# Optimization experiments

Measured on AMD Instinct MI355X. Metric: run time of the kernel, lower is better.

The kernel has to match this reference:

```python
import jax, jax.numpy as jnp
import numpy as np

N = 8192       # num nodes
D_IN = 256     # in_features
D_OUT = 128    # out_features per head
H = 2          # num_heads
E = 262144     # num edges (avg degree 32)
ALPHA = 0.2    # leaky relu slope


def setup_inputs() -> dict:
    key = jax.random.key(0)
    k1, k2, k3, k4 = jax.random.split(key, 4)
    x = jax.random.normal(k1, (N, D_IN), dtype=jnp.float32)
    # per-head Linear weights: W[h] is [out, in] (y = x @ W.T), a[h] is [2*out]
    W = jax.random.normal(k2, (H, D_OUT, D_IN), dtype=jnp.float32) * (1.0 / np.sqrt(D_IN))
    a = jax.random.normal(k3, (H, 2 * D_OUT), dtype=jnp.float32) * (1.0 / np.sqrt(2 * D_OUT))
    edge_index = jax.random.randint(k4, (2, E), 0, N, dtype=jnp.int32)
    return {"x": x, "W": W, "a": a, "edge_index": edge_index}


def reference(x, W, a, edge_index):
    # h[h,n,d] = W(x) per head
    h = jnp.einsum('nf,hdf->hnd', x, W)
    # a([h_i ; h_j]) decomposes into a_src . h_i + a_dst . h_j
    a_src, a_dst = a[:, :D_OUT], a[:, D_OUT:]
    s_i = jnp.einsum('hnd,hd->hn', h, a_src)
    s_j = jnpp_dummy = None
    s_j = jnp.einsum('hnd,hd->hn', h, a_dst)
    score = s_i[:, :, None] + s_j[:, None, :]  # [H, n, n]
    # dense adjacency mask from edge list
    adj = jnp.zeros((N, N), dtype=jnp.bool_).at[edge_index[0], edge_index[1]].set(True)
    # faithful to original: non-edges set to 0 (NOT -inf) before leaky_relu + softmax
    e = jnp.where(adj[None, :, :], score, jnp.float32(0.0))
    e = jnp.where(e > 0, e, ALPHA * e)  # leaky relu
    att = jax.nn.softmax(e, axis=-1)    # softmax over j (dim=1 of original [n,n])
    out = jnp.einsum('hij,hjd->hid', att, h)  # aggregate: attention @ h
    out = jnp.transpose(out, (1, 0, 2)).reshape(N, H * D_OUT)  # concat heads
    return jax.nn.elu(out)
```

## Files before the change

### kernel.cpp

```cpp
#include <hip/hip_runtime.h>
#include <hip/hip_bf16.h>

#define N_NODES 8192
#define DIN     256
#define DOUT    128
#define NHEAD   2
#define CTOT    256
#define NWORDS  256
#define LRELU_A 0.2f
#define CAP     512
#define LDR     40

typedef __attribute__((ext_vector_type(8))) short bf16x8;
typedef __attribute__((ext_vector_type(4))) float f32x4;

__device__ __forceinline__ float bf(unsigned short u) {
    return __uint_as_float((unsigned)u << 16);
}
__device__ __forceinline__ unsigned short f2bf(float f) {
    unsigned u = __float_as_uint(f);
    u = (u + 0x7fffu + ((u >> 16) & 1u)) >> 16;
    return (unsigned short)u;
}
__device__ __forceinline__ unsigned pk(float a, float b) {
    return (unsigned)f2bf(a) | ((unsigned)f2bf(b) << 16);
}

__global__ __launch_bounds__(256) void k_pre(const float* __restrict__ x,
                                             const float* __restrict__ W,
                                             const float* __restrict__ a,
                                             unsigned short* __restrict__ hb16,
                                             float* __restrict__ sp_src,
                                             float* __restrict__ sp_dst,
                                             float4* __restrict__ adjp,
                                             float4* __restrict__ sallp) {
    __shared__ unsigned short As[64 * LDR];
    __shared__ unsigned short Bs[64 * LDR];
    int b = blockIdx.x, t = threadIdx.x;

    if (b == 2560) {
        if (t < 64) sallp[t] = make_float4(0.f, 0.f, 0.f, 0.f);
        return;
    }
    if (b >= 512) {
        adjp[(b - 512) * 256 + t] = make_float4(0.f, 0.f, 0.f, 0.f);
        return;
    }

    int bm = (b & 127) * 64;
    int bn = (b >> 7) * 64;
    int wv = t >> 6, lane = t & 63;
    int fr = lane & 15, ksl = lane >> 4;

    f32x4 acc[4] = {};
    for (int k0 = 0; k0 < DIN; k0 += 32) {
        {
            int row = t >> 2, slot = t & 3;
            const float4* srcA = reinterpret_cast<const float4*>(&x[(bm + row) * DIN + k0 + slot * 8]);
            float4 va0 = srcA[0], va1 = srcA[1];
            *reinterpret_cast<uint4*>(&As[row * LDR + slot * 8]) =
                make_uint4(pk(va0.x, va0.y), pk(va0.z, va0.w), pk(va1.x, va1.y), pk(va1.z, va1.w));
            const float4* srcB = reinterpret_cast<const float4*>(&W[(bn + row) * DIN + k0 + slot * 8]);
            float4 vb0 = srcB[0], vb1 = srcB[1];
            *reinterpret_cast<uint4*>(&Bs[row * LDR + slot * 8]) =
                make_uint4(pk(vb0.x, vb0.y), pk(vb0.z, vb0.w), pk(vb1.x, vb1.y), pk(vb1.z, vb1.w));
        }
        __syncthreads();
        bf16x8 af = *reinterpret_cast<const bf16x8*>(&As[(wv * 16 + fr) * LDR + ksl * 8]);
        #pragma unroll
        for (int fn = 0; fn < 4; ++fn) {
            bf16x8 bfr = *reinterpret_cast<const bf16x8*>(&Bs[(fn * 16 + fr) * LDR + ksl * 8]);
            acc[fn] = __builtin_amdgcn_mfma_f32_16x16x32_bf16(af, bfr, acc[fn], 0, 0, 0);
        }
        __syncthreads();
    }

    #pragma unroll
    for (int fn = 0; fn < 4; ++fn) {
        int c = bn + fn * 16 + fr;
        int r0 = bm + wv * 16 + ksl * 4;
        #pragma unroll
        for (int r = 0; r < 4; ++r)
            hb16[(size_t)(r0 + r) * CTOT + c] = f2bf(acc[fn][r]);
    }

    int head = (bn >= 128);
    int q    = bn >> 6;
    float as[4], ad[4];
    #pragma unroll
    for (int fn = 0; fn < 4; ++fn) {
        int d = (bn & 127) + fn * 16 + fr;
        as[fn] = a[head * 256 + d];
        ad[fn] = a[head * 256 + 128 + d];
    }
    #pragma unroll
    for (int r = 0; r < 4; ++r) {
        float ps = acc[0][r] * as[0] + acc[1][r] * as[1] + acc[2][r] * as[2] + acc[3][r] * as[3];
        float pd = acc[0][r] * ad[0] + acc[1][r] * ad[1] + acc[2][r] * ad[2] + acc[3][r] * ad[3];
        #pragma unroll
        for (int off = 8; off; off >>= 1) {
            ps += __shfl_xor(ps, off);
            pd += __shfl_xor(pd, off);
        }
        if (fr == 0) {
            int row = bm + wv * 16 + ksl * 4 + r;
            sp_src[q * N_NODES + row] = ps;
            sp_dst[q * N_NODES + row] = pd;
        }
    }
}

__global__ __launch_bounds__(256) void k_mid(const int* __restrict__ ei, int E,
                                             unsigned int* __restrict__ adjw,
                                             const float* __restrict__ sp_src,
                                             const float* __restrict__ sp_dst,
                                             const unsigned short* __restrict__ hb16,
                                             float* __restrict__ s_src,
                                             float* __restrict__ s_dst,
                                             float* __restrict__ S_all) {
    int b = blockIdx.x, t = threadIdx.x;

    if (b < 1024) {
        int e = b * 256 + t;
        if (e < E) {
            int src = ei[e];
            int dst = ei[E + e];
            atomicOr(&adjw[(size_t)src * NWORDS + (dst >> 5)], 1u << (dst & 31));
        }
        return;
    }
    if (b < 1056) {
        int n = (b - 1024) * 256 + t;
        s_src[n]           = sp_src[0 * N_NODES + n] + sp_src[1 * N_NODES + n];
        s_src[N_NODES + n] = sp_src[2 * N_NODES + n] + sp_src[3 * N_NODES + n];
        s_dst[n]           = sp_dst[0 * N_NODES + n] + sp_dst[1 * N_NODES + n];
        s_dst[N_NODES + n] = sp_dst[2 * N_NODES + n] + sp_dst[3 * N_NODES + n];
        return;
    }

    int r0 = (b - 1056) * 16;
    float s = 0.f;
    #pragma unroll
    for (int r = r0; r < r0 + 16; ++r)
        s += bf(hb16[r * CTOT + t]);
    atomicAdd(&S_all[t], s);
}

__global__ __launch_bounds__(256) void k_attn(const unsigned int* __restrict__ adjw,
                                              const float* __restrict__ s_src,
                                              const float* __restrict__ s_dst,
                                              const unsigned short* __restrict__ hb16,
                                              const float* __restrict__ S_all,
                                              float* __restrict__ out) {
    __shared__ unsigned short nbr[CAP];
    __shared__ float          ew0[CAP];
    __shared__ float          ew1[CAP];
    __shared__ int            wtot[4];
    __shared__ float          zr0[4];
    __shared__ float          zr1[4];

    int i    = blockIdx.x;
    int t    = threadIdx.x;
    int lane = t & 63;
    int wv   = t >> 6;

    unsigned int w = adjw[(size_t)i * NWORDS + t];
    int cnt = __popc(w);
    int inc = cnt;
    #pragma unroll
    for (int off = 1; off < 64; off <<= 1) {
        int v = __shfl_up(inc, off);
        if (lane >= off) inc += v;
    }
    if (lane == 63) wtot[wv] = inc;
    __syncthreads();
    int base = 0;
    #pragma unroll
    for (int q = 0; q < 3; ++q) if (q < wv) base += wtot[q];
    int deg = wtot[0] + wtot[1] + wtot[2] + wtot[3];
    int pos = base + inc - cnt;
    unsigned int ww = w;
    while (ww) {
        int bb = __ffs(ww) - 1;
        ww &= ww - 1;
        if (pos < CAP) nbr[pos] = (unsigned short)(t * 32 + bb);
        ++pos;
    }
    if (deg > CAP) deg = CAP;
    __syncthreads();

    float ss0 = s_src[i], ss1 = s_src[N_NODES + i];
    float z0 = 0.f, z1 = 0.f;
    for (int k = t; k < deg; k += 256) {
        int j = nbr[k];
        float v0 = ss0 + s_dst[j];
        float v1 = ss1 + s_dst[N_NODES + j];
        float e0 = v0 > 0.f ? v0 : LRELU_A * v0;
        float e1 = v1 > 0.f ? v1 : LRELU_A * v1;
        float w0 = expf(e0) - 1.f;
        float w1 = expf(e1) - 1.f;
        ew0[k] = w0; ew1[k] = w1;
        z0 += w0; z1 += w1;
    }
    #pragma unroll
    for (int off = 32; off; off >>= 1) {
        z0 += __shfl_xor(z0, off);
        z1 += __shfl_xor(z1, off);
    }
    if (lane == 0) { zr0[wv] = z0; zr1[wv] = z1; }
    __syncthreads();
    float Z0 = (float)N_NODES + zr0[0] + zr0[1] + zr0[2] + zr0[3];
    float Z1 = (float)N_NODES + zr1[0] + zr1[1] + zr1[2] + zr1[3];

    int hh = t >> 7;
    const float* ewh = hh ? ew1 : ew0;
    float Zh = hh ? Z1 : Z0;
    float acc = 0.f;
    int k = 0;
    for (; k + 8 <= deg; k += 8) {
        int j0 = nbr[k+0], j1 = nbr[k+1], j2 = nbr[k+2], j3 = nbr[k+3];
        int j4 = nbr[k+4], j5 = nbr[k+5], j6 = nbr[k+6], j7 = nbr[k+7];
        float w0 = ewh[k+0], w1 = ewh[k+1], w2 = ewh[k+2], w3 = ewh[k+3];
        float w4 = ewh[k+4], w5 = ewh[k+5], w6 = ewh[k+6], w7 = ewh[k+7];
        float v0 = bf(hb16[j0 * CTOT + t]);
        float v1 = bf(hb16[j1 * CTOT + t]);
        float v2 = bf(hb16[j2 * CTOT + t]);
        float v3 = bf(hb16[j3 * CTOT + t]);
        float v4 = bf(hb16[j4 * CTOT + t]);
        float v5 = bf(hb16[j5 * CTOT + t]);
        float v6 = bf(hb16[j6 * CTOT + t]);
        float v7 = bf(hb16[j7 * CTOT + t]);
        acc = fmaf(w0, v0, acc); acc = fmaf(w1, v1, acc);
        acc = fmaf(w2, v2, acc); acc = fmaf(w3, v3, acc);
        acc = fmaf(w4, v4, acc); acc = fmaf(w5, v5, acc);
        acc = fmaf(w6, v6, acc); acc = fmaf(w7, v7, acc);
    }
    for (; k + 4 <= deg; k += 4) {
        int j0 = nbr[k], j1 = nbr[k+1], j2 = nbr[k+2], j3 = nbr[k+3];
        float w0 = ewh[k], w1 = ewh[k+1], w2 = ewh[k+2], w3 = ewh[k+3];
        float v0 = bf(hb16[j0 * CTOT + t]);
        float v1 = bf(hb16[j1 * CTOT + t]);
        float v2 = bf(hb16[j2 * CTOT + t]);
        float v3 = bf(hb16[j3 * CTOT + t]);
        acc = fmaf(w0, v0, acc); acc = fmaf(w1, v1, acc);
        acc = fmaf(w2, v2, acc); acc = fmaf(w3, v3, acc);
    }
    for (; k < deg; ++k)
        acc = fmaf(ewh[k], bf(hb16[nbr[k] * CTOT + t]), acc);

    float o = (S_all[t] + acc) / Zh;
    o = o > 0.f ? o : expm1f(o);
    out[i * CTOT + t] = o;
}

extern "C" void kernel_launch(void* const* d_in, const int* in_sizes, int n_in,
                              void* d_out, int out_size, void* d_ws, size_t ws_size,
                              hipStream_t stream) {
    const float* x  = (const float*)d_in[0];
    const float* W  = (const float*)d_in[1];
    const float* a  = (const float*)d_in[2];
    const int*   ei = (const int*)d_in[3];
    int E = in_sizes[3] / 2;
    float* out = (float*)d_out;

    char* ws = (char*)d_ws;
    size_t off = 0;
    auto alloc = [&](size_t bytes) { char* p = ws + off; off += (bytes + 255) & ~(size_t)255; return p; };
    unsigned int*   adjw   = (unsigned int*)  alloc((size_t)N_NODES * NWORDS * 4);
    float*          S_all  = (float*)         alloc(CTOT * 4);
    float*          s_src  = (float*)         alloc((size_t)NHEAD * N_NODES * 4);
    float*          s_dst  = (float*)         alloc((size_t)NHEAD * N_NODES * 4);
    unsigned short* hb16   = (unsigned short*)alloc((size_t)N_NODES * CTOT * 2);
    float*          sp_src = (float*)         alloc((size_t)4 * N_NODES * 4);
    float*          sp_dst = (float*)         alloc((size_t)4 * N_NODES * 4);

    k_pre<<<2561, 256, 0, stream>>>(x, W, a, hb16, sp_src, sp_dst, (float4*)adjw, (float4*)S_all);
    k_mid<<<1568, 256, 0, stream>>>(ei, E, adjw, sp_src, sp_dst, hb16, s_src, s_dst, S_all);
    k_attn<<<N_NODES, 256, 0, stream>>>(adjw, s_src, s_dst, hb16, S_all, out);
}
```

Measured before the change: 66.32 us.

## Make each wave build its own neighbor list and drop block barriers in attention

Each of the four waves in the attention kernel now scans the full adjacency row itself, using 16-byte loads, and builds a private neighbor list and edge-weight array with wave-level scans and reductions. This removes all __syncthreads and shared cross-wave reductions, and each wave computes weights for only its own head. The cost is redundant compaction work across waves and a smaller neighbor cap of 128, which could truncate high-degree rows. With random edges averaging degree 32, overflow is unlikely.

```diff
diff --git a/kernel.cpp b/kernel.cpp
--- a/kernel.cpp
+++ b/kernel.cpp
@@ -8,7 +8,7 @@
 #define CTOT    256
 #define NWORDS  256
 #define LRELU_A 0.2f
-#define CAP     512
+#define CAPN    128
 #define LDR     40
 
 typedef __attribute__((ext_vector_type(8))) short bf16x8;
@@ -152,105 +152,88 @@
                                               const unsigned short* __restrict__ hb16,
                                               const float* __restrict__ S_all,
                                               float* __restrict__ out) {
-    __shared__ unsigned short nbr[CAP];
-    __shared__ float          ew0[CAP];
-    __shared__ float          ew1[CAP];
-    __shared__ int            wtot[4];
-    __shared__ float          zr0[4];
-    __shared__ float          zr1[4];
+    __shared__ unsigned short nbr[4][CAPN];
+    __shared__ float          ewl[4][CAPN];
 
     int i    = blockIdx.x;
     int t    = threadIdx.x;
+    int wv   = t >> 6;
     int lane = t & 63;
-    int wv   = t >> 6;
-
-    unsigned int w = adjw[(size_t)i * NWORDS + t];
-    int cnt = __popc(w);
+    int head = wv >> 1;
+    int c    = wv * 64 + lane;
+
+    const uint4 wq = reinterpret_cast<const uint4*>(adjw + (size_t)i * NWORDS)[lane];
+    int cnt = __popc(wq.x) + __popc(wq.y) + __popc(wq.z) + __popc(wq.w);
     int inc = cnt;
     #pragma unroll
     for (int off = 1; off < 64; off <<= 1) {
         int v = __shfl_up(inc, off);
         if (lane >= off) inc += v;
     }
-    if (lane == 63) wtot[wv] = inc;
-    __syncthreads();
-    int base = 0;
-    #pragma unroll
-    for (int q = 0; q < 3; ++q) if (q < wv) base += wtot[q];
-    int deg = wtot[0] + wtot[1] + wtot[2] + wtot[3];
-    int pos = base + inc - cnt;
-    unsigned int ww = w;
-    while (ww) {
-        int bb = __ffs(ww) - 1;
-        ww &= ww - 1;
-        if (pos < CAP) nbr[pos] = (unsigned short)(t * 32 + bb);
-        ++pos;
-    }
-    if (deg > CAP) deg = CAP;
-    __syncthreads();
-
-    float ss0 = s_src[i], ss1 = s_src[N_NODES + i];
-    float z0 = 0.f, z1 = 0.f;
-    for (int k = t; k < deg; k += 256) {
-        int j = nbr[k];
-        float v0 = ss0 + s_dst[j];
-        float v1 = ss1 + s_dst[N_NODES + j];
-        float e0 = v0 > 0.f ? v0 : LRELU_A * v0;
-        float e1 = v1 > 0.f ? v1 : LRELU_A * v1;
-        float w0 = expf(e0) - 1.f;
-        float w1 = expf(e1) - 1.f;
-        ew0[k] = w0; ew1[k] = w1;
-        z0 += w0; z1 += w1;
-    }
-    #pragma unroll
-    for (int off = 32; off; off >>= 1) {
-        z0 += __shfl_xor(z0, off);
-        z1 += __shfl_xor(z1, off);
-    }
-    if (lane == 0) { zr0[wv] = z0; zr1[wv] = z1; }
-    __syncthreads();
-    float Z0 = (float)N_NODES + zr0[0] + zr0[1] + zr0[2] + zr0[3];
-    float Z1 = (float)N_NODES + zr1[0] + zr1[1] + zr1[2] + zr1[3];
-
-    int hh = t >> 7;
-    const float* ewh = hh ? ew1 : ew0;
-    float Zh = hh ? Z1 : Z0;
+    int deg = __shfl(inc, 63);
+    int pos = inc - cnt;
+    int idb = lane * 128;
+    {
+        unsigned int w;
+        w = wq.x; while (w) { int bb = __ffs(w) - 1; w &= w - 1; if (pos < CAPN) nbr[wv][pos] = (unsigned short)(idb + bb);      ++pos; }
+        w = wq.y; while (w) { int bb = __ffs(w) - 1; w &= w - 1; if (pos < CAPN) nbr[wv][pos] = (unsigned short)(idb + 32 + bb); ++pos; }
+        w = wq.z; while (w) { int bb = __ffs(w) - 1; w &= w - 1; if (pos < CAPN) nbr[wv][pos] = (unsigned short)(idb + 64 + bb); ++pos; }
+        w = wq.w; while (w) { int bb = __ffs(w) - 1; w &= w - 1; if (pos < CAPN) nbr[wv][pos] = (unsigned short)(idb + 96 + bb); ++pos; }
+    }
+    if (deg > CAPN) deg = CAPN;
+
+    float ssh = s_src[head * N_NODES + i];
+    const float* sdh = s_dst + head * N_NODES;
+    float z = 0.f;
+    for (int k = lane; k < deg; k += 64) {
+        int j = nbr[wv][k];
+        float v = ssh + sdh[j];
+        float e = v > 0.f ? v : LRELU_A * v;
+        float w = expf(e) - 1.f;
+        ewl[wv][k] = w;
+        z += w;
+    }
+    #pragma unroll
+    for (int off = 32; off; off >>= 1)
+        z += __shfl_xor(z, off);
+    float Z = (float)N_NODES + z;
+
     float acc = 0.f;
     int k = 0;
     for (; k + 8 <= deg; k += 8) {
-        int j0 = nbr[k+0], j1 = nbr[k+1], j2 = nbr[k+2], j3 = nbr[k+3];
-        int j4 = nbr[k+4], j5 = nbr[k+5], j6 = nbr[k+6], j7 = nbr[k+7];
-        float w0 = ewh[k+0], w1 = ewh[k+1], w2 = ewh[k+2], w3 = ewh[k+3];
-        float w4 = ewh[k+4], w5 = ewh[k+5], w6 = ewh[k+6], w7 = ewh[k+7];
-        float v0 = bf(hb16[j0 * CTOT + t]);
-        float v1 = bf(hb16[j1 * CTOT + t]);
-        float v2 = bf(hb16[j2 * CTOT + t]);
-        float v3 = bf(hb16[j3 * CTOT + t]);
-        float v4 = bf(hb16[j4 * CTOT + t]);
-        float v5 = bf(hb16[j5 * CTOT + t]);
-        float v6 = bf(hb16[j6 * CTOT + t]);
-        float v7 = bf(hb16[j7 * CTOT + t]);
+        int j0 = nbr[wv][k+0], j1 = nbr[wv][k+1], j2 = nbr[wv][k+2], j3 = nbr[wv][k+3];
+        int j4 = nbr[wv][k+4], j5 = nbr[wv][k+5], j6 = nbr[wv][k+6], j7 = nbr[wv][k+7];
+        float w0 = ewl[wv][k+0], w1 = ewl[wv][k+1], w2 = ewl[wv][k+2], w3 = ewl[wv][k+3];
+        float w4 = ewl[wv][k+4], w5 = ewl[wv][k+5], w6 = ewl[wv][k+6], w7 = ewl[wv][k+7];
+        float v0 = bf(hb16[j0 * CTOT + c]);
+        float v1 = bf(hb16[j1 * CTOT + c]);
+        float v2 = bf(hb16[j2 * CTOT + c]);
+        float v3 = bf(hb16[j3 * CTOT + c]);
+        float v4 = bf(hb16[j4 * CTOT + c]);
+        float v5 = bf(hb16[j5 * CTOT + c]);
+        float v6 = bf(hb16[j6 * CTOT + c]);
+        float v7 = bf(hb16[j7 * CTOT + c]);
         acc = fmaf(w0, v0, acc); acc = fmaf(w1, v1, acc);
         acc = fmaf(w2, v2, acc); acc = fmaf(w3, v3, acc);
         acc = fmaf(w4, v4, acc); acc = fmaf(w5, v5, acc);
         acc = fmaf(w6, v6, acc); acc = fmaf(w7, v7, acc);
     }
     for (; k + 4 <= deg; k += 4) {
-        int j0 = nbr[k], j1 = nbr[k+1], j2 = nbr[k+2], j3 = nbr[k+3];
-        float w0 = ewh[k], w1 = ewh[k+1], w2 = ewh[k+2], w3 = ewh[k+3];
-        float v0 = bf(hb16[j0 * CTOT + t]);
-        float v1 = bf(hb16[j1 * CTOT + t]);
-        float v2 = bf(hb16[j2 * CTOT + t]);
-        float v3 = bf(hb16[j3 * CTOT + t]);
+        int j0 = nbr[wv][k], j1 = nbr[wv][k+1], j2 = nbr[wv][k+2], j3 = nbr[wv][k+3];
+        float w0 = ewl[wv][k], w1 = ewl[wv][k+1], w2 = ewl[wv][k+2], w3 = ewl[wv][k+3];
+        float v0 = bf(hb16[j0 * CTOT + c]);
+        float v1 = bf(hb16[j1 * CTOT + c]);
+        float v2 = bf(hb16[j2 * CTOT + c]);
+        float v3 = bf(hb16[j3 * CTOT + c]);
         acc = fmaf(w0, v0, acc); acc = fmaf(w1, v1, acc);
         acc = fmaf(w2, v2, acc); acc = fmaf(w3, v3, acc);
     }
     for (; k < deg; ++k)
-        acc = fmaf(ewh[k], bf(hb16[nbr[k] * CTOT + t]), acc);
-
-    float o = (S_all[t] + acc) / Zh;
+        acc = fmaf(ewl[wv][k], bf(hb16[nbr[wv][k] * CTOT + c]), acc);
+
+    float o = (S_all[c] + acc) / Z;
     o = o > 0.f ? o : expm1f(o);
-    out[i * CTOT + t] = o;
+    out[i * CTOT + c] = o;
 }
 
 extern "C" void kernel_launch(void* const* d_in, const int* in_sizes, int n_in,
```

After: 67.43 us. Within noise of the previous version (+1.7%).
